# Kernel optimization log

Hardware: AMD Instinct MI355X
Metric: run time of the kernel (lower is better)

## Reference

```python
import jax, jax.numpy as jnp
import numpy as np

TOP_K = 2  # hard-coded in MoCo.__init__ (self.top_k = 2)


def setup_inputs() -> dict:
    key = jax.random.key(0)
    k1, k2, k3 = jax.random.split(key, 3)
    B, D, E, O = 16384, 4096, 4, 256  # batch, mlp_dim, num_experts, dim
    v_standard = jax.random.normal(k1, (B, D), dtype=jnp.float32)
    router_w = jax.random.normal(k2, (D, E), dtype=jnp.float32) / np.float32(np.sqrt(D))
    expert_w = jax.random.normal(k3, (E, D, O), dtype=jnp.float32) / np.float32(np.sqrt(D))
    return {"v_standard": v_standard, "router_w": router_w, "expert_w": expert_w}


def reference(v_standard, router_w, expert_w):
    # Router + softmax gating: [B, E]
    routing_logits = v_standard @ router_w
    routing_weights = jax.nn.softmax(routing_logits, axis=-1)

    # Top-k gating, renormalized over the selected experts
    topk_weights, topk_indices = jax.lax.top_k(routing_weights, TOP_K)  # [B, k]
    topk_weights = topk_weights / topk_weights.sum(axis=-1, keepdims=True)

    # Dense all-expert compute (as in the original: every expert runs on every token)
    expert_outputs = jnp.einsum('bd,edo->beo', v_standard, expert_w)  # [B, E, O]

    # Gather the top-k expert outputs and combine with gate weights
    selected = jnp.take_along_axis(expert_outputs, topk_indices[:, :, None], axis=1)  # [B, k, O]
    moe_output = (selected * topk_weights[:, :, None]).sum(axis=1)  # [B, O]
    return moe_output, routing_weights
```

## Files before the change

kernel.cpp:

```cpp
#include <hip/hip_runtime.h>

typedef unsigned short ushort_t;
typedef __attribute__((ext_vector_type(8))) short short8;
typedef __attribute__((ext_vector_type(4))) float floatx4;
typedef __attribute__((ext_vector_type(4))) unsigned int uint4v;

static __device__ __forceinline__ unsigned short f2bf_rn(float f) {
  return (unsigned short)((__float_as_uint(f) + 0x8000u) >> 16);
}
static __device__ __forceinline__ unsigned int packbf(float a, float b) {
  return ((__float_as_uint(a) + 0x8000u) >> 16) |
         ((__float_as_uint(b) + 0x8000u) & 0xFFFF0000u);
}
static __device__ __forceinline__ void gld_lds16(const void* g, void* l) {
  __builtin_amdgcn_global_load_lds(
      (const __attribute__((address_space(1))) unsigned int*)g,
      (__attribute__((address_space(3))) unsigned int*)l, 16, 0, 0);
}

__global__ __launch_bounds__(256) void k_transpose(const float* __restrict__ We,
                                                   ushort_t* __restrict__ WT) {
  __shared__ float tile[32][33];
  int t = threadIdx.x, tx = t & 31, ty = t >> 5;
  int d0 = blockIdx.x * 32, o0 = blockIdx.y * 32, e = blockIdx.z;
  const float* src = We + (size_t)e * 4096 * 256;
  ushort_t* dst = WT + (size_t)e * 256 * 4096;
#pragma unroll
  for (int r = 0; r < 4; ++r)
    tile[ty + r * 8][tx] = src[(size_t)(d0 + ty + r * 8) * 256 + (o0 + tx)];
  __syncthreads();
#pragma unroll
  for (int r = 0; r < 4; ++r)
    dst[(size_t)(o0 + ty + r * 8) * 4096 + (d0 + tx)] = f2bf_rn(tile[tx][ty + r * 8]);
}

__global__ __launch_bounds__(256) void k_prep_router(const float* __restrict__ Wr,
                                                     float* __restrict__ WrT32) {
  int d = blockIdx.x * 256 + threadIdx.x;
  float4 w = *(const float4*)(Wr + (size_t)d * 4);
  WrT32[d] = w.x;
  WrT32[4096 + d] = w.y;
  WrT32[2 * 4096 + d] = w.z;
  WrT32[3 * 4096 + d] = w.w;
}

__global__ __launch_bounds__(256) void k_routing2(const float* __restrict__ V,
                                                  const float* __restrict__ WrT32,
                                                  float* __restrict__ rw_out,
                                                  float* __restrict__ gates,
                                                  ushort_t* __restrict__ Vh) {
  int w = threadIdx.x >> 6, lane = threadIdx.x & 63;
  int b = blockIdx.x * 4 + w;
  const float* vrow = V + (size_t)b * 4096;
  ushort_t* vhrow = Vh + (size_t)b * 4096;
  float a0 = 0.f, a1 = 0.f, a2 = 0.f, a3 = 0.f;
#pragma unroll 4
  for (int j = 0; j < 16; ++j) {
    int d = j * 256 + lane * 4;
    float4 vv = *(const float4*)(vrow + d);
    float4 w0 = *(const float4*)(WrT32 + d);
    float4 w1 = *(const float4*)(WrT32 + 4096 + d);
    float4 w2 = *(const float4*)(WrT32 + 2 * 4096 + d);
    float4 w3 = *(const float4*)(WrT32 + 3 * 4096 + d);
    a0 += vv.x * w0.x + vv.y * w0.y + vv.z * w0.z + vv.w * w0.w;
    a1 += vv.x * w1.x + vv.y * w1.y + vv.z * w1.z + vv.w * w1.w;
    a2 += vv.x * w2.x + vv.y * w2.y + vv.z * w2.z + vv.w * w2.w;
    a3 += vv.x * w3.x + vv.y * w3.y + vv.z * w3.z + vv.w * w3.w;
    uint2 pk;
    pk.x = packbf(vv.x, vv.y);
    pk.y = packbf(vv.z, vv.w);
    *(uint2*)(vhrow + d) = pk;
  }
#pragma unroll
  for (int mask = 1; mask < 64; mask <<= 1) {
    a0 += __shfl_xor(a0, mask, 64);
    a1 += __shfl_xor(a1, mask, 64);
    a2 += __shfl_xor(a2, mask, 64);
    a3 += __shfl_xor(a3, mask, 64);
  }
  float mx = fmaxf(fmaxf(a0, a1), fmaxf(a2, a3));
  float e0 = expf(a0 - mx), e1 = expf(a1 - mx), e2 = expf(a2 - mx), e3 = expf(a3 - mx);
  float s = e0 + e1 + e2 + e3;
  float p[4] = {e0 / s, e1 / s, e2 / s, e3 / s};
  int i1 = 0;
#pragma unroll
  for (int k = 1; k < 4; ++k)
    if (p[k] > p[i1]) i1 = k;
  int i2 = (i1 == 0) ? 1 : 0;
#pragma unroll
  for (int k = 0; k < 4; ++k)
    if (k != i1 && p[k] > p[i2]) i2 = k;
  float gs = p[i1] + p[i2];
  if (lane < 4) {
    rw_out[(size_t)b * 4 + lane] = p[lane];
    gates[(size_t)b * 4 + lane] = (lane == i1 || lane == i2) ? (p[lane] / gs) : 0.f;
  }
}

#define BM2 128
#define BN2 64
#define BK2 64

__global__ __launch_bounds__(512, 4) void k_gemm2(const ushort_t* __restrict__ Vh,
                                                  const ushort_t* __restrict__ WT,
                                                  const float* __restrict__ gates,
                                                  float* __restrict__ out) {
  const int Kd = 4096;
  int g = blockIdx.x;
  int xcd = g & 7, slot = g >> 3;
  int bm = xcd + ((slot >> 2) << 3);
  int bn = slot & 3;
  int m0 = bm * BM2, n0 = bn * BN2;

  __shared__ __align__(16) ushort_t Asm[BM2 * BK2];
  __shared__ __align__(16) ushort_t Bsm[4 * BN2 * BK2];

  int t = threadIdx.x;
  int w = t >> 6, lane = t & 63;
  int quad = lane >> 4, mi = lane & 15;
  int wm = (w >> 2) * 64;
  int wn = (w & 3) * 16;

  size_t aSrc[2];
  int aDst[2];
#pragma unroll
  for (int s = 0; s < 2; ++s) {
    int q = (w * 2 + s) * 64 + lane;
    int row = q >> 3, c = (q & 7) ^ (row & 7);
    aSrc[s] = (size_t)(m0 + row) * Kd + c * 8;
    aDst[s] = (w * 2 + s) * 512;
  }
  size_t bSrc[4];
  int bDst[4];
#pragma unroll
  for (int s = 0; s < 4; ++s) {
    int q = (w * 4 + s) * 64 + lane;
    int e = q >> 9, r = (q >> 3) & 63, c = (q & 7) ^ (r & 7);
    bSrc[s] = (size_t)e * 256 * Kd + (size_t)(n0 + r) * Kd + c * 8;
    bDst[s] = (w * 4 + s) * 512;
  }

  int aOff[2][4], bOff[2];
#pragma unroll
  for (int k32 = 0; k32 < 2; ++k32) {
    int cc = k32 * 4 + quad;
#pragma unroll
    for (int i = 0; i < 4; ++i) {
      int ra = wm + i * 16 + mi;
      aOff[k32][i] = (ra * 8 + (cc ^ (ra & 7))) * 8;
    }
    int rb = wn + mi;
    bOff[k32] = (rb * 8 + (cc ^ (rb & 7))) * 8;
  }

  floatx4 zero = {0.f, 0.f, 0.f, 0.f};
  floatx4 acc[4][4];
#pragma unroll
  for (int e = 0; e < 4; ++e)
#pragma unroll
    for (int i = 0; i < 4; ++i) acc[e][i] = zero;

  for (int kt = 0; kt < Kd / BK2; ++kt) {
    size_t k0 = (size_t)kt * BK2;
#pragma unroll
    for (int s = 0; s < 2; ++s) gld_lds16(Vh + aSrc[s] + k0, Asm + aDst[s]);
#pragma unroll
    for (int s = 0; s < 4; ++s) gld_lds16(WT + bSrc[s] + k0, Bsm + bDst[s]);
    __syncthreads();

#pragma unroll
    for (int k32 = 0; k32 < 2; ++k32) {
      short8 af[4];
#pragma unroll
      for (int i = 0; i < 4; ++i) af[i] = *(const short8*)(Asm + aOff[k32][i]);
#pragma unroll
      for (int e = 0; e < 4; ++e) {
        short8 bfr = *(const short8*)(Bsm + e * (BN2 * BK2) + bOff[k32]);
#pragma unroll
        for (int i = 0; i < 4; ++i)
          acc[e][i] =
              __builtin_amdgcn_mfma_f32_16x16x32_bf16(af[i], bfr, acc[e][i], 0, 0, 0);
      }
    }
    __syncthreads();
  }

#pragma unroll
  for (int i = 0; i < 4; ++i) {
#pragma unroll
    for (int r = 0; r < 4; ++r) {
      int m = m0 + wm + i * 16 + quad * 4 + r;
      float4 gv = *(const float4*)(gates + (size_t)m * 4);
      float sv = gv.x * acc[0][i][r] + gv.y * acc[1][i][r] +
                 gv.z * acc[2][i][r] + gv.w * acc[3][i][r];
      out[(size_t)m * 256 + n0 + wn + mi] = sv;
    }
  }
}

__global__ __launch_bounds__(256) void k_routing(const float* __restrict__ V,
                                                 const float* __restrict__ WrT32,
                                                 float* __restrict__ rw_out,
                                                 float* __restrict__ gates) {
  int w = threadIdx.x >> 6, lane = threadIdx.x & 63;
  int b = blockIdx.x * 4 + w;
  const float* vrow = V + (size_t)b * 4096;
  float a0 = 0.f, a1 = 0.f, a2 = 0.f, a3 = 0.f;
#pragma unroll
  for (int j = 0; j < 16; ++j) {
    int d = j * 256 + lane * 4;
    float4 vv = *(const float4*)(vrow + d);
    float4 w0 = *(const float4*)(WrT32 + d);
    float4 w1 = *(const float4*)(WrT32 + 4096 + d);
    float4 w2 = *(const float4*)(WrT32 + 2 * 4096 + d);
    float4 w3 = *(const float4*)(WrT32 + 3 * 4096 + d);
    a0 += vv.x * w0.x + vv.y * w0.y + vv.z * w0.z + vv.w * w0.w;
    a1 += vv.x * w1.x + vv.y * w1.y + vv.z * w1.z + vv.w * w1.w;
    a2 += vv.x * w2.x + vv.y * w2.y + vv.z * w2.z + vv.w * w2.w;
    a3 += vv.x * w3.x + vv.y * w3.y + vv.z * w3.z + vv.w * w3.w;
  }
#pragma unroll
  for (int mask = 1; mask < 64; mask <<= 1) {
    a0 += __shfl_xor(a0, mask, 64);
    a1 += __shfl_xor(a1, mask, 64);
    a2 += __shfl_xor(a2, mask, 64);
    a3 += __shfl_xor(a3, mask, 64);
  }
  float mx = fmaxf(fmaxf(a0, a1), fmaxf(a2, a3));
  float e0 = expf(a0 - mx), e1 = expf(a1 - mx), e2 = expf(a2 - mx), e3 = expf(a3 - mx);
  float s = e0 + e1 + e2 + e3;
  float p[4] = {e0 / s, e1 / s, e2 / s, e3 / s};
  int i1 = 0;
#pragma unroll
  for (int k = 1; k < 4; ++k)
    if (p[k] > p[i1]) i1 = k;
  int i2 = (i1 == 0) ? 1 : 0;
#pragma unroll
  for (int k = 0; k < 4; ++k)
    if (k != i1 && p[k] > p[i2]) i2 = k;
  float gs = p[i1] + p[i2];
  if (lane < 4) {
    rw_out[(size_t)b * 4 + lane] = p[lane];
    gates[(size_t)b * 4 + lane] = (lane == i1 || lane == i2) ? (p[lane] / gs) : 0.f;
  }
}

#define BM 128
#define BN 64
#define BK 64

__global__ __launch_bounds__(256, 2) void k_gemm_moe(const float* __restrict__ V,
                                                     const ushort_t* __restrict__ WT,
                                                     const float* __restrict__ gates,
                                                     float* __restrict__ out) {
  const int Kd = 4096;
  int bn = blockIdx.x;
  int bm = blockIdx.y;
  int m0 = bm * BM, n0 = bn * BN;

  __shared__ __align__(16) ushort_t Asm[BM * BK];
  __shared__ __align__(16) ushort_t Bsm[4 * BN * BK];

  int t = threadIdx.x;
  int w = t >> 6, lane = t & 63;
  int quad = lane >> 4, mi = lane & 15;
  int wm = (w >> 1) * 64, wn = (w & 1) * 32;

  int aG[4], aL[4];
#pragma unroll
  for (int j = 0; j < 4; ++j) {
    int q = j * 256 + t;
    int row = q >> 3, c = q & 7;
    aG[j] = (m0 + row) * Kd + c * 8;
    aL[j] = (row * 8 + (c ^ (row & 7))) * 8;
  }
  int bG[8], bL[8];
#pragma unroll
  for (int j = 0; j < 8; ++j) {
    int q = j * 256 + t;
    int eb = q >> 9, rc = q & 511;
    int r = rc >> 3, c = rc & 7;
    bG[j] = eb * (256 * Kd) + (n0 + r) * Kd + c * 8;
    bL[j] = eb * (BN * BK) + (r * 8 + (c ^ (r & 7))) * 8;
  }

  int aOff[2][4], bOff[2][2];
#pragma unroll
  for (int k32 = 0; k32 < 2; ++k32) {
    int cc = k32 * 4 + quad;
#pragma unroll
    for (int i = 0; i < 4; ++i) {
      int rowa = wm + i * 16 + mi;
      aOff[k32][i] = (rowa * 8 + (cc ^ (rowa & 7))) * 8;
    }
#pragma unroll
    for (int j = 0; j < 2; ++j) {
      int rowb = wn + j * 16 + mi;
      bOff[k32][j] = (rowb * 8 + (cc ^ (rowb & 7))) * 8;
    }
  }

  floatx4 zero = {0.f, 0.f, 0.f, 0.f};
  floatx4 acc[4][4][2];
#pragma unroll
  for (int e = 0; e < 4; ++e)
#pragma unroll
    for (int i = 0; i < 4; ++i)
#pragma unroll
      for (int j = 0; j < 2; ++j) acc[e][i][j] = zero;

  float4 ax[4], ay[4];
  short8 bv[8];
#pragma unroll
  for (int j = 0; j < 4; ++j) {
    const float* ap = V + (size_t)aG[j];
    ax[j] = *(const float4*)ap;
    ay[j] = *(const float4*)(ap + 4);
  }
#pragma unroll
  for (int j = 0; j < 8; ++j) bv[j] = *(const short8*)(WT + (size_t)bG[j]);

  for (int kt = 0; kt < Kd / BK; ++kt) {
#pragma unroll
    for (int j = 0; j < 4; ++j) {
      uint4v uv;
      uv.x = packbf(ax[j].x, ax[j].y);
      uv.y = packbf(ax[j].z, ax[j].w);
      uv.z = packbf(ay[j].x, ay[j].y);
      uv.w = packbf(ay[j].z, ay[j].w);
      *(uint4v*)(Asm + aL[j]) = uv;
    }
#pragma unroll
    for (int j = 0; j < 8; ++j) *(short8*)(Bsm + bL[j]) = bv[j];
    __syncthreads();

    if (kt + 1 < Kd / BK) {
      int k0n = (kt + 1) * BK;
#pragma unroll
      for (int j = 0; j < 4; ++j) {
        const float* ap = V + (size_t)(aG[j] + k0n);
        ax[j] = *(const float4*)ap;
        ay[j] = *(const float4*)(ap + 4);
      }
#pragma unroll
      for (int j = 0; j < 8; ++j) bv[j] = *(const short8*)(WT + (size_t)(bG[j] + k0n));
    }

#pragma unroll
    for (int k32 = 0; k32 < 2; ++k32) {
      short8 af[4];
#pragma unroll
      for (int i = 0; i < 4; ++i) af[i] = *(const short8*)(Asm + aOff[k32][i]);
#pragma unroll
      for (int e = 0; e < 4; ++e) {
        short8 bfr[2];
#pragma unroll
        for (int j = 0; j < 2; ++j)
          bfr[j] = *(const short8*)(Bsm + e * (BN * BK) + bOff[k32][j]);
#pragma unroll
        for (int i = 0; i < 4; ++i)
#pragma unroll
          for (int j = 0; j < 2; ++j)
            acc[e][i][j] =
                __builtin_amdgcn_mfma_f32_16x16x32_bf16(af[i], bfr[j], acc[e][i][j], 0, 0, 0);
      }
    }
    __syncthreads();
  }

#pragma unroll
  for (int i = 0; i < 4; ++i) {
#pragma unroll
    for (int r = 0; r < 4; ++r) {
      int m = m0 + wm + i * 16 + quad * 4 + r;
      float4 gv = *(const float4*)(gates + (size_t)m * 4);
#pragma unroll
      for (int j = 0; j < 2; ++j) {
        float sv = gv.x * acc[0][i][j][r] + gv.y * acc[1][i][j][r] +
                   gv.z * acc[2][i][j][r] + gv.w * acc[3][i][j][r];
        out[(size_t)m * 256 + n0 + wn + j * 16 + mi] = sv;
      }
    }
  }
}

extern "C" void kernel_launch(void* const* d_in, const int* in_sizes, int n_in,
                              void* d_out, int out_size, void* d_ws, size_t ws_size,
                              hipStream_t stream) {
  const float* V = (const float*)d_in[0];
  const float* Wr = (const float*)d_in[1];
  const float* We = (const float*)d_in[2];

  float* out_moe = (float*)d_out;
  float* out_rw = out_moe + (size_t)16384 * 256;

  char* ws = (char*)d_ws;
  float* gates = (float*)ws;
  ushort_t* WT = (ushort_t*)(ws + 262144);
  float* WrT32 = (float*)(ws + 262144 + 8388608);
  ushort_t* Vh = (ushort_t*)(ws + 262144 + 8388608 + 65536);
  size_t need = 262144ull + 8388608ull + 65536ull + 16384ull * 4096ull * 2ull;

  k_transpose<<<dim3(128, 8, 4), 256, 0, stream>>>(We, WT);
  k_prep_router<<<dim3(16), 256, 0, stream>>>(Wr, WrT32);

  if (ws_size >= need) {
    k_routing2<<<dim3(4096), 256, 0, stream>>>(V, WrT32, out_rw, gates, Vh);
    k_gemm2<<<dim3(512), 512, 0, stream>>>(Vh, WT, gates, out_moe);
  } else {
    k_routing<<<dim3(4096), 256, 0, stream>>>(V, WrT32, out_rw, gates);
    k_gemm_moe<<<dim3(4, 128), 256, 0, stream>>>(V, WT, gates, out_moe);
  }
}
```

Measured before the change: 525.5 us.

## Double-buffer LDS tiles in expert GEMM and raise MFMA wave priority

Splits the A/B shared-memory tiles into two buffers so the global-to-LDS loads for the next K step are issued before the MFMAs on the current step. This overlaps memory latency with compute and drops one barrier per iteration. It also wraps the MFMA block in s_setprio to favour compute waves. Doubling LDS use lowers the occupancy hint from 4 to 2 blocks per CU.

Result: slower. 600.3 us (+14.2%).

```diff
diff --git a/kernel.cpp b/kernel.cpp
--- a/kernel.cpp
+++ b/kernel.cpp
@@ -100,20 +100,23 @@
 #define BM2 128
 #define BN2 64
 #define BK2 64
-
-__global__ __launch_bounds__(512, 4) void k_gemm2(const ushort_t* __restrict__ Vh,
+#define ASZ (BM2 * BK2)
+#define BSZ (4 * BN2 * BK2)
+
+__global__ __launch_bounds__(512, 2) void k_gemm2(const ushort_t* __restrict__ Vh,
                                                   const ushort_t* __restrict__ WT,
                                                   const float* __restrict__ gates,
                                                   float* __restrict__ out) {
   const int Kd = 4096;
+  const int NT = Kd / BK2;
   int g = blockIdx.x;
   int xcd = g & 7, slot = g >> 3;
   int bm = xcd + ((slot >> 2) << 3);
   int bn = slot & 3;
   int m0 = bm * BM2, n0 = bn * BN2;
 
-  __shared__ __align__(16) ushort_t Asm[BM2 * BK2];
-  __shared__ __align__(16) ushort_t Bsm[4 * BN2 * BK2];
+  __shared__ __align__(16) ushort_t Asm[2 * ASZ];
+  __shared__ __align__(16) ushort_t Bsm[2 * BSZ];
 
   int t = threadIdx.x;
   int w = t >> 6, lane = t & 63;
@@ -160,29 +163,45 @@
 #pragma unroll
     for (int i = 0; i < 4; ++i) acc[e][i] = zero;
 
-  for (int kt = 0; kt < Kd / BK2; ++kt) {
-    size_t k0 = (size_t)kt * BK2;
-#pragma unroll
-    for (int s = 0; s < 2; ++s) gld_lds16(Vh + aSrc[s] + k0, Asm + aDst[s]);
-#pragma unroll
-    for (int s = 0; s < 4; ++s) gld_lds16(WT + bSrc[s] + k0, Bsm + bDst[s]);
-    __syncthreads();
-
+#pragma unroll
+  for (int s = 0; s < 2; ++s) gld_lds16(Vh + aSrc[s], Asm + aDst[s]);
+#pragma unroll
+  for (int s = 0; s < 4; ++s) gld_lds16(WT + bSrc[s], Bsm + bDst[s]);
+  __syncthreads();
+
+  int cur = 0;
+  for (int kt = 0; kt < NT; ++kt) {
+    int nxt = cur ^ 1;
+    if (kt + 1 < NT) {
+      size_t k0n = (size_t)(kt + 1) * BK2;
+#pragma unroll
+      for (int s = 0; s < 2; ++s)
+        gld_lds16(Vh + aSrc[s] + k0n, Asm + nxt * ASZ + aDst[s]);
+#pragma unroll
+      for (int s = 0; s < 4; ++s)
+        gld_lds16(WT + bSrc[s] + k0n, Bsm + nxt * BSZ + bDst[s]);
+    }
+
+    const ushort_t* Ab = Asm + cur * ASZ;
+    const ushort_t* Bb = Bsm + cur * BSZ;
 #pragma unroll
     for (int k32 = 0; k32 < 2; ++k32) {
       short8 af[4];
 #pragma unroll
-      for (int i = 0; i < 4; ++i) af[i] = *(const short8*)(Asm + aOff[k32][i]);
+      for (int i = 0; i < 4; ++i) af[i] = *(const short8*)(Ab + aOff[k32][i]);
+      __builtin_amdgcn_s_setprio(1);
 #pragma unroll
       for (int e = 0; e < 4; ++e) {
-        short8 bfr = *(const short8*)(Bsm + e * (BN2 * BK2) + bOff[k32]);
+        short8 bfr = *(const short8*)(Bb + e * (BN2 * BK2) + bOff[k32]);
 #pragma unroll
         for (int i = 0; i < 4; ++i)
           acc[e][i] =
               __builtin_amdgcn_mfma_f32_16x16x32_bf16(af[i], bfr, acc[e][i], 0, 0, 0);
       }
+      __builtin_amdgcn_s_setprio(0);
     }
     __syncthreads();
+    cur = nxt;
   }
 
 #pragma unroll
```
